# Performance work log

Hardware: AMD Instinct MI355X
Metric: run time of the kernel (lower is better)

## Reference

```python
import jax, jax.numpy as jnp
import numpy as np
from jax import lax

C = 128        # args.feat_dim
HF = WF = 320  # feature map spatial size
IMG = 1280     # segmentation map resolution
N = 256        # number of anchors
CROP = 32      # fixed crop size (h and w)
NUM_CLASSES = 151
NUM_BASE = 64


def setup_inputs() -> dict:
    key = jax.random.key(0)
    ks = jax.random.split(key, 9)
    feature_map = jax.random.normal(ks[0], (C, HF, WF), dtype=jnp.float32)
    seg = jax.random.randint(ks[1], (IMG, IMG), 0, NUM_CLASSES, dtype=jnp.int32)
    x0 = jax.random.randint(ks[2], (N,), 0, WF - CROP, dtype=jnp.int32)
    y0 = jax.random.randint(ks[3], (N,), 0, HF - CROP, dtype=jnp.int32)
    # anchors layout matches torch code: [x0, x1, y0, y1] in feature-map pixels
    anchors = jnp.stack([x0, x0 + CROP, y0, y0 + CROP], axis=1)
    labels = jax.random.randint(ks[4], (N,), 0, NUM_BASE, dtype=jnp.int32)
    base_classes = jax.random.randint(ks[5], (NUM_BASE,), 0, NUM_CLASSES, dtype=jnp.int32)
    W1 = jax.random.normal(ks[6], (256, C, 3, 3), dtype=jnp.float32) * 0.02
    b1 = jnp.zeros((256,), dtype=jnp.float32)
    W2 = jax.random.normal(ks[7], (1, 256, 3, 3), dtype=jnp.float32) * 0.02
    b2 = jnp.zeros((1,), dtype=jnp.float32)
    return {"feature_map": feature_map, "seg": seg, "anchors": anchors,
            "labels": labels, "base_classes": base_classes,
            "W1": W1, "b1": b1, "W2": W2, "b2": b2}


def reference(feature_map, seg, anchors, labels, base_classes, W1, b1, W2, b2):
    # F.interpolate(mode='nearest') from IMGxIMG down to HFxWF: idx = floor(i * in/out)
    hi = (jnp.arange(HF) * seg.shape[0]) // HF
    wi = (jnp.arange(WF) * seg.shape[1]) // WF
    mask = seg[hi][:, wi].astype(jnp.float32)  # [HF, WF]

    starts = anchors[:, jnp.array([2, 0])]  # (h0, w0) per anchor

    def crop_feat(s):
        return lax.dynamic_slice(feature_map, (jnp.int32(0), s[0], s[1]), (C, CROP, CROP))

    def crop_mask(s):
        return lax.dynamic_slice(mask, (s[0], s[1]), (CROP, CROP))

    crops = jax.vmap(crop_feat)(starts)       # [N, C, CROP, CROP]
    mask_crops = jax.vmap(crop_mask)(starts)  # [N, CROP, CROP]

    dn = ('NCHW', 'OIHW', 'NCHW')
    h = lax.conv_general_dilated(crops, W1, (1, 1), 'SAME', dimension_numbers=dn)
    h = jax.nn.relu(h + b1[None, :, None, None])
    logits = lax.conv_general_dilated(h, W2, (1, 1), 'SAME', dimension_numbers=dn)
    logits = logits + b2[None, :, None, None]  # [N, 1, CROP, CROP]

    tgt_cls = base_classes[labels].astype(jnp.float32)  # [N]
    tgt = (mask_crops == tgt_cls[:, None, None]).astype(jnp.float32)[:, None]  # [N,1,CROP,CROP]

    # stable BCE-with-logits: max(x,0) - x*t + log1p(exp(-|x|))
    bce = jnp.maximum(logits, 0.0) - logits * tgt + jnp.log1p(jnp.exp(-jnp.abs(logits)))
    per_anchor = bce.mean(axis=(1, 2, 3))  # mean per anchor, as in F.binary_cross_entropy_with_logits
    return per_anchor.sum() / (N + 1e-10)
```

## Files before the change

### kernel.cpp

```cpp
#include <hip/hip_runtime.h>

typedef __attribute__((ext_vector_type(8))) short short8;
typedef __attribute__((ext_vector_type(8))) int int8v;
typedef __attribute__((ext_vector_type(16))) float floatx16;
typedef __attribute__((ext_vector_type(4))) unsigned int uint4v;
typedef unsigned short ushort_t;
typedef unsigned int uint_t;
typedef unsigned char uchar_t;

#define NA   256
#define CIN  128
#define HFD  320
#define FMPX (HFD*HFD)
#define IMGD 1280

#define W1B_BYTE_OFF (1u<<20)
#define W2R_BYTE_OFF ((1u<<20) + 9*256*128)
#define FMT_BYTE_OFF (2u<<20)

#define SAPL 5440
#define SA_BYTES (4*SAPL)
#define PSTR_H 4112
#define SMEM_BYTES (8*PSTR_H)

union V32 { int8v v; uint4v q[2]; };

__device__ __forceinline__ ushort_t f2bf(float v) {
    uint_t u = __float_as_uint(v);
    return (ushort_t)((u + 0x8000u) >> 16);
}
__device__ __forceinline__ uchar_t f2fp8(float v) {
    int r = __builtin_amdgcn_cvt_pk_fp8_f32(v, 0.0f, 0, false);
    return (uchar_t)(r & 0xff);
}

__global__ __launch_bounds__(256) void prep_kernel(
    const float* __restrict__ fm, const float* __restrict__ W1, const float* __restrict__ W2,
    float* __restrict__ logits, float* __restrict__ out,
    uchar_t* __restrict__ w1b, ushort_t* __restrict__ w2r, uchar_t* __restrict__ fmT)
{
    const int b = blockIdx.x, t = threadIdx.x;
    if (b < 3200) {
        if (b < 1024) logits[b * 256 + t] = 0.0f;
        __shared__ uchar_t s[32 * 144];
        const int y = b / 10, x0b = (b % 10) * 32;
        #pragma unroll
        for (int i = 0; i < 16; ++i) {
            int e = t + 256 * i;
            int c = e >> 5, xo = e & 31;
            s[xo * 144 + c] = f2fp8(fm[(size_t)c * FMPX + y * HFD + x0b + xo]);
        }
        __syncthreads();
        int xo = t >> 3, cg = t & 7;
        uint4v v = *(const uint4v*)&s[xo * 144 + cg * 16];
        *(uint4v*)&fmT[((size_t)(y * HFD + x0b + xo)) * 128 + cg * 16] = v;
    } else if (b < 3328) {
        int e = (b - 3200) * 256 + t;
        int oc = e >> 7, cin = e & 127;
        int g = oc >> 6, nt = (oc >> 5) & 1, l = oc & 31;
        int cb = cin >> 6, kh = (cin >> 5) & 1, byte = cin & 31;
        int dst = cb * 147456 + g * 4096 + nt * 2048 + (l * 2 + kh) * 32 + byte;
        #pragma unroll
        for (int tap = 0; tap < 9; ++tap)
            w1b[dst + tap * 16384] = f2fp8(W1[(oc * 128 + cin) * 9 + tap] * 64.0f);
    } else {
        #pragma unroll
        for (int i = 0; i < 32; ++i) {
            int e = i * 256 + t;
            int nrow = e >> 8, oc = e & 255;
            w2r[nrow * 256 + oc] = f2bf(nrow < 9 ? W2[oc * 9 + nrow] : 0.0f);
        }
        if (t == 0) out[0] = 0.0f;
    }
}

__global__ __launch_bounds__(256, 2) void conv_mfma_kernel(
    const int* __restrict__ anchors, const uchar_t* __restrict__ fmT,
    const uchar_t* __restrict__ w1b, const ushort_t* __restrict__ w2r,
    const float* __restrict__ b1, float* __restrict__ logits)
{
    const int id  = blockIdx.x;
    const int xcd = id & 7, sid = id >> 3;
    const int n   = xcd * 32 + (sid >> 4);
    const int rem = sid & 15;
    const int q   = rem >> 2;
    const int g   = rem & 3;

    const int t    = threadIdx.x;
    const int w    = t >> 6;
    const int lane = t & 63;
    const int l31  = lane & 31;
    const int kh   = lane >> 5;

    const int x0 = anchors[n * 4 + 0];
    const int y0 = anchors[n * 4 + 2];
    const int r0 = q * 8;

    __shared__ __align__(16) char smem[SMEM_BYTES];
    __shared__ float s_log[10 * 32];

    for (int i = t; i < SA_BYTES / 4; i += 256) ((uint_t*)smem)[i] = 0u;

    floatx16 acc[2][2];
    #pragma unroll
    for (int mt = 0; mt < 2; ++mt)
        #pragma unroll
        for (int nt = 0; nt < 2; ++nt)
            #pragma unroll
            for (int r = 0; r < 16; ++r) acc[mt][nt][r] = 0.0f;

    const uchar_t* w1g = w1b + (size_t)(g * 4096) + (l31 * 2 + kh) * 32;

    for (int c = 0; c < 2; ++c) {
        const int cb = c * 64;
        __syncthreads();
        #pragma unroll
        for (int j = 0; j < 5; ++j) {
            int u = t + 256 * j;
            int sub = u & 3, cell = u >> 2;
            int col = cell & 31, pr = cell >> 5;
            int cr = r0 + pr - 1;
            if ((unsigned)cr < 32u) {
                uint4v v = *(const uint4v*)&fmT[((size_t)((y0 + cr) * HFD + x0 + col)) * 128 + cb + sub * 16];
                *(uint4v*)(smem + sub * SAPL + (pr * 34 + col + 1) * 16) = v;
            }
        }
        __syncthreads();
        const uchar_t* w1c = w1g + c * 147456;
        #pragma unroll
        for (int kx = 0; kx < 3; ++kx) {
            V32 a8[4];
            #pragma unroll
            for (int idx = 0; idx < 4; ++idx) {
                int cell = (2 * w + idx) * 34 + l31 + kx;
                a8[idx].q[0] = *(const uint4v*)(smem + (2 * kh)     * SAPL + cell * 16);
                a8[idx].q[1] = *(const uint4v*)(smem + (2 * kh + 1) * SAPL + cell * 16);
            }
            #pragma unroll
            for (int ky = 0; ky < 3; ++ky) {
                const int tap = ky * 3 + kx;
                V32 b8[2];
                #pragma unroll
                for (int nt = 0; nt < 2; ++nt) {
                    const uchar_t* bp = w1c + tap * 16384 + nt * 2048;
                    b8[nt].q[0] = *(const uint4v*)bp;
                    b8[nt].q[1] = *(const uint4v*)(bp + 16);
                }
                #pragma unroll
                for (int mt = 0; mt < 2; ++mt) {
                    acc[mt][0] = __builtin_amdgcn_mfma_scale_f32_32x32x64_f8f6f4(
                        a8[mt + ky].v, b8[0].v, acc[mt][0], 0, 0, 0, 127, 0, 127);
                    acc[mt][1] = __builtin_amdgcn_mfma_scale_f32_32x32x64_f8f6f4(
                        a8[mt + ky].v, b8[1].v, acc[mt][1], 0, 0, 0, 127, 0, 127);
                }
            }
        }
    }

    __syncthreads();
    #pragma unroll
    for (int nt = 0; nt < 2; ++nt) {
        float bias = b1[g * 64 + nt * 32 + l31];
        int plane = nt * 4 + (l31 >> 3);
        #pragma unroll
        for (int mt = 0; mt < 2; ++mt) {
            int lr = 2 * w + mt;
            #pragma unroll
            for (int reg = 0; reg < 16; ++reg) {
                int col = (reg & 3) + 8 * (reg >> 2) + 4 * kh;
                float hv = fmaxf(fmaf(acc[mt][nt][reg], 0.015625f, bias), 0.0f);
                *(ushort_t*)(smem + plane * PSTR_H + ((lr * 32 + col) * 8 + (l31 & 7)) * 2) = f2bf(hv);
            }
        }
    }
    __syncthreads();

    floatx16 vacc[2];
    #pragma unroll
    for (int mt = 0; mt < 2; ++mt)
        #pragma unroll
        for (int r = 0; r < 16; ++r) vacc[mt][r] = 0.0f;
    #pragma unroll
    for (int ks = 0; ks < 4; ++ks) {
        short8 bw = *(const short8*)&w2r[l31 * 256 + g * 64 + ks * 16 + kh * 8];
        #pragma unroll
        for (int mt = 0; mt < 2; ++mt) {
            short8 ah = *(const short8*)(smem + (ks * 2 + kh) * PSTR_H + ((2 * w + mt) * 32 + l31) * 16);
            vacc[mt] = __builtin_amdgcn_mfma_f32_32x32x16_bf16(ah, bw, vacc[mt], 0, 0, 0);
        }
    }

    __syncthreads();
    for (int i = t; i < 10 * 32; i += 256) s_log[i] = 0.0f;
    __syncthreads();
    if (l31 < 9) {
        int ky = l31 / 3, kx = l31 - ky * 3;
        #pragma unroll
        for (int mt = 0; mt < 2; ++mt) {
            int outr = 2 * w + mt + 2 - ky;
            #pragma unroll
            for (int reg = 0; reg < 16; ++reg) {
                int col  = (reg & 3) + 8 * (reg >> 2) + 4 * kh;
                int outc = col + 1 - kx;
                if (outc >= 0 && outc < 32)
                    atomicAdd(&s_log[outr * 32 + outc], vacc[mt][reg]);
            }
        }
    }
    __syncthreads();
    for (int i = t; i < 10 * 32; i += 256) {
        int outr = i >> 5, outc = i & 31;
        int R = r0 + outr - 1;
        if ((unsigned)R < 32u)
            atomicAdd(&logits[n * 1024 + R * 32 + outc], s_log[i]);
    }
}

__global__ __launch_bounds__(256) void bce_reduce_kernel(
    const float* __restrict__ logits, const int* __restrict__ seg,
    const int* __restrict__ anchors, const int* __restrict__ labels,
    const int* __restrict__ base_classes, const float* __restrict__ b2,
    float* __restrict__ out)
{
    const int n = blockIdx.x;
    const int t = threadIdx.x;
    const int y0 = anchors[n * 4 + 2];
    const int x0 = anchors[n * 4 + 0];
    const int tgt_cls = base_classes[labels[n]];
    const float bias2 = b2[0];

    float lsum = 0.0f;
    #pragma unroll
    for (int r = 0; r < 4; ++r) {
        int p = t + r * 256;
        int i = p >> 5, j = p & 31;
        float l = logits[n * 1024 + p] + bias2;
        int sv = seg[(size_t)(4 * (y0 + i)) * IMGD + 4 * (x0 + j)];
        float tgt = (sv == tgt_cls) ? 1.0f : 0.0f;
        lsum += fmaxf(l, 0.0f) - l * tgt + log1pf(expf(-fabsf(l)));
    }
    #pragma unroll
    for (int off = 32; off > 0; off >>= 1) lsum += __shfl_down(lsum, off, 64);
    __shared__ float s[4];
    if ((t & 63) == 0) s[t >> 6] = lsum;
    __syncthreads();
    if (t == 0) {
        float tot = s[0] + s[1] + s[2] + s[3];
        const float scale = 1.0f / (1024.0f * (256.0f + 1e-10f));
        atomicAdd(out, tot * scale);
    }
}

extern "C" void kernel_launch(void* const* d_in, const int* in_sizes, int n_in,
                              void* d_out, int out_size, void* d_ws, size_t ws_size,
                              hipStream_t stream) {
    const float* fm           = (const float*)d_in[0];
    const int*   seg          = (const int*)d_in[1];
    const int*   anchors      = (const int*)d_in[2];
    const int*   labels       = (const int*)d_in[3];
    const int*   base_classes = (const int*)d_in[4];
    const float* W1           = (const float*)d_in[5];
    const float* b1           = (const float*)d_in[6];
    const float* W2           = (const float*)d_in[7];
    const float* b2           = (const float*)d_in[8];
    float* out = (float*)d_out;

    float*    logits = (float*)d_ws;
    uchar_t*  w1b    = (uchar_t*)((char*)d_ws + W1B_BYTE_OFF);
    ushort_t* w2r    = (ushort_t*)((char*)d_ws + W2R_BYTE_OFF);
    uchar_t*  fmT    = (uchar_t*)((char*)d_ws + FMT_BYTE_OFF);

    prep_kernel<<<3329, 256, 0, stream>>>(fm, W1, W2, logits, out, w1b, w2r, fmT);
    conv_mfma_kernel<<<4096, 256, 0, stream>>>(anchors, fmT, w1b, w2r, b1, logits);
    bce_reduce_kernel<<<NA, 256, 0, stream>>>(logits, seg, anchors, labels, base_classes, b2, out);
}
```

Measured before the change: 256.2 us.

## Split conv1 output channels into 8 groups and stage weights in LDS

Each block now computes 32 output channels instead of 64, doubling the grid to 8192 blocks. W1 is re-laid out so each block's per-chunk weight slice is copied into shared memory and read from there, instead of being fetched from global memory for every tap. The padded A tile is replaced by an unpadded one, with edge columns zeroed in registers. The aim is fewer accumulators, more parallelism and cheaper B-operand loads. In exchange, the input tile load is duplicated across twice as many blocks and more shared memory is used.

```diff
diff --git a/kernel.cpp b/kernel.cpp
--- a/kernel.cpp
+++ b/kernel.cpp
@@ -18,10 +18,12 @@
 #define W2R_BYTE_OFF ((1u<<20) + 9*256*128)
 #define FMT_BYTE_OFF (2u<<20)
 
-#define SAPL 5440
+#define SAPL 5120
 #define SA_BYTES (4*SAPL)
+#define SBPL 4608
+#define SB_BYTES (4*SBPL)
+#define SMEM_BYTES (SA_BYTES + SB_BYTES)
 #define PSTR_H 4112
-#define SMEM_BYTES (8*PSTR_H)
 
 union V32 { int8v v; uint4v q[2]; };
 
@@ -57,12 +59,12 @@
     } else if (b < 3328) {
         int e = (b - 3200) * 256 + t;
         int oc = e >> 7, cin = e & 127;
-        int g = oc >> 6, nt = (oc >> 5) & 1, l = oc & 31;
-        int cb = cin >> 6, kh = (cin >> 5) & 1, byte = cin & 31;
-        int dst = cb * 147456 + g * 4096 + nt * 2048 + (l * 2 + kh) * 32 + byte;
+        int g = oc >> 5, ocl = oc & 31;
+        int cb = cin >> 6, sub = (cin >> 4) & 3, b16 = cin & 15;
+        size_t dst = ((size_t)((cb * 8 + g) * 4 + sub)) * 4608 + ocl * 16 + b16;
         #pragma unroll
         for (int tap = 0; tap < 9; ++tap)
-            w1b[dst + tap * 16384] = f2fp8(W1[(oc * 128 + cin) * 9 + tap] * 64.0f);
+            w1b[dst + tap * 512] = f2fp8(W1[(oc * 128 + cin) * 9 + tap] * 64.0f);
     } else {
         #pragma unroll
         for (int i = 0; i < 32; ++i) {
@@ -81,10 +83,10 @@
 {
     const int id  = blockIdx.x;
     const int xcd = id & 7, sid = id >> 3;
-    const int n   = xcd * 32 + (sid >> 4);
-    const int rem = sid & 15;
-    const int q   = rem >> 2;
-    const int g   = rem & 3;
+    const int n   = xcd * 32 + (sid >> 5);
+    const int rem = sid & 31;
+    const int q   = rem >> 3;
+    const int g   = rem & 7;
 
     const int t    = threadIdx.x;
     const int w    = t >> 6;
@@ -98,18 +100,17 @@
 
     __shared__ __align__(16) char smem[SMEM_BYTES];
     __shared__ float s_log[10 * 32];
+    char* sb = smem + SA_BYTES;
 
     for (int i = t; i < SA_BYTES / 4; i += 256) ((uint_t*)smem)[i] = 0u;
 
-    floatx16 acc[2][2];
+    floatx16 acc[2];
     #pragma unroll
     for (int mt = 0; mt < 2; ++mt)
         #pragma unroll
-        for (int nt = 0; nt < 2; ++nt)
-            #pragma unroll
-            for (int r = 0; r < 16; ++r) acc[mt][nt][r] = 0.0f;
-
-    const uchar_t* w1g = w1b + (size_t)(g * 4096) + (l31 * 2 + kh) * 32;
+        for (int r = 0; r < 16; ++r) acc[mt][r] = 0.0f;
+
+    const uint4v vzero = {0u, 0u, 0u, 0u};
 
     for (int c = 0; c < 2; ++c) {
         const int cb = c * 64;
@@ -118,57 +119,62 @@
         for (int j = 0; j < 5; ++j) {
             int u = t + 256 * j;
             int sub = u & 3, cell = u >> 2;
-            int col = cell & 31, pr = cell >> 5;
-            int cr = r0 + pr - 1;
+            int col = cell & 31, row = cell >> 5;
+            int cr = r0 + row - 1;
             if ((unsigned)cr < 32u) {
                 uint4v v = *(const uint4v*)&fmT[((size_t)((y0 + cr) * HFD + x0 + col)) * 128 + cb + sub * 16];
-                *(uint4v*)(smem + sub * SAPL + (pr * 34 + col + 1) * 16) = v;
+                *(uint4v*)(smem + sub * SAPL + cell * 16) = v;
+            }
+        }
+        const uchar_t* wsrc = w1b + (size_t)((c * 8 + g)) * 18432;
+        #pragma unroll
+        for (int j = 0; j < 5; ++j) {
+            int u = t + 256 * j;
+            if (u < 1152) {
+                uint4v v = *(const uint4v*)(wsrc + u * 16);
+                *(uint4v*)(sb + u * 16) = v;
             }
         }
         __syncthreads();
-        const uchar_t* w1c = w1g + c * 147456;
         #pragma unroll
         for (int kx = 0; kx < 3; ++kx) {
             V32 a8[4];
             #pragma unroll
             for (int idx = 0; idx < 4; ++idx) {
-                int cell = (2 * w + idx) * 34 + l31 + kx;
-                a8[idx].q[0] = *(const uint4v*)(smem + (2 * kh)     * SAPL + cell * 16);
-                a8[idx].q[1] = *(const uint4v*)(smem + (2 * kh + 1) * SAPL + cell * 16);
+                int cell = (2 * w + idx) * 32 + l31 + kx - 1;
+                int cc = cell < 0 ? 0 : cell;
+                a8[idx].q[0] = *(const uint4v*)(smem + (2 * kh)     * SAPL + cc * 16);
+                a8[idx].q[1] = *(const uint4v*)(smem + (2 * kh + 1) * SAPL + cc * 16);
+            }
+            if ((kx == 0 && l31 == 0) || (kx == 2 && l31 == 31)) {
+                #pragma unroll
+                for (int idx = 0; idx < 4; ++idx) { a8[idx].q[0] = vzero; a8[idx].q[1] = vzero; }
             }
             #pragma unroll
             for (int ky = 0; ky < 3; ++ky) {
-                const int tap = ky * 3 + kx;
-                V32 b8[2];
+                int cellb = (ky * 3 + kx) * 32 + l31;
+                V32 b8;
+                b8.q[0] = *(const uint4v*)(sb + (2 * kh)     * SBPL + cellb * 16);
+                b8.q[1] = *(const uint4v*)(sb + (2 * kh + 1) * SBPL + cellb * 16);
                 #pragma unroll
-                for (int nt = 0; nt < 2; ++nt) {
-                    const uchar_t* bp = w1c + tap * 16384 + nt * 2048;
-                    b8[nt].q[0] = *(const uint4v*)bp;
-                    b8[nt].q[1] = *(const uint4v*)(bp + 16);
-                }
-                #pragma unroll
-                for (int mt = 0; mt < 2; ++mt) {
-                    acc[mt][0] = __builtin_amdgcn_mfma_scale_f32_32x32x64_f8f6f4(
-                        a8[mt + ky].v, b8[0].v, acc[mt][0], 0, 0, 0, 127, 0, 127);
-                    acc[mt][1] = __builtin_amdgcn_mfma_scale_f32_32x32x64_f8f6f4(
-                        a8[mt + ky].v, b8[1].v, acc[mt][1], 0, 0, 0, 127, 0, 127);
-                }
-            }
-        }
-    }
-
-    __syncthreads();
-    #pragma unroll
-    for (int nt = 0; nt < 2; ++nt) {
-        float bias = b1[g * 64 + nt * 32 + l31];
-        int plane = nt * 4 + (l31 >> 3);
+                for (int mt = 0; mt < 2; ++mt)
+                    acc[mt] = __builtin_amdgcn_mfma_scale_f32_32x32x64_f8f6f4(
+                        a8[mt + ky].v, b8.v, acc[mt], 0, 0, 0, 127, 0, 127);
+            }
+        }
+    }
+
+    __syncthreads();
+    {
+        float bias = b1[g * 32 + l31];
+        int plane = l31 >> 3;
         #pragma unroll
         for (int mt = 0; mt < 2; ++mt) {
             int lr = 2 * w + mt;
             #pragma unroll
             for (int reg = 0; reg < 16; ++reg) {
                 int col = (reg & 3) + 8 * (reg >> 2) + 4 * kh;
-                float hv = fmaxf(fmaf(acc[mt][nt][reg], 0.015625f, bias), 0.0f);
+                float hv = fmaxf(fmaf(acc[mt][reg], 0.015625f, bias), 0.0f);
                 *(ushort_t*)(smem + plane * PSTR_H + ((lr * 32 + col) * 8 + (l31 & 7)) * 2) = f2bf(hv);
             }
         }
@@ -181,8 +187,8 @@
         #pragma unroll
         for (int r = 0; r < 16; ++r) vacc[mt][r] = 0.0f;
     #pragma unroll
-    for (int ks = 0; ks < 4; ++ks) {
-        short8 bw = *(const short8*)&w2r[l31 * 256 + g * 64 + ks * 16 + kh * 8];
+    for (int ks = 0; ks < 2; ++ks) {
+        short8 bw = *(const short8*)&w2r[l31 * 256 + g * 32 + ks * 16 + kh * 8];
         #pragma unroll
         for (int mt = 0; mt < 2; ++mt) {
             short8 ah = *(const short8*)(smem + (ks * 2 + kh) * PSTR_H + ((2 * w + mt) * 32 + l31) * 16);
@@ -271,6 +277,6 @@
     uchar_t*  fmT    = (uchar_t*)((char*)d_ws + FMT_BYTE_OFF);
 
     prep_kernel<<<3329, 256, 0, stream>>>(fm, W1, W2, logits, out, w1b, w2r, fmT);
-    conv_mfma_kernel<<<4096, 256, 0, stream>>>(anchors, fmT, w1b, w2r, b1, logits);
+    conv_mfma_kernel<<<8192, 256, 0, stream>>>(anchors, fmT, w1b, w2r, b1, logits);
     bce_reduce_kernel<<<NA, 256, 0, stream>>>(logits, seg, anchors, labels, base_classes, b2, out);
 }
```

New measurement: 326.5 us. +27.4%, slower.
